# Kernel tuning notes

Measured on AMD Instinct MI355X. Metric: run time of the kernel, lower is better.

Reference implementation:

```python
import jax, jax.numpy as jnp
import numpy as np

B = 4_194_304
N_LAYERS = 2


def setup_inputs() -> dict:
    key = jax.random.key(0)
    k1, k2 = jax.random.split(key)
    x = jax.random.normal(k1, (B, 2), dtype=jnp.float32)
    q_weights = 0.01 * jax.random.normal(k2, (N_LAYERS, 2), dtype=jnp.float32)
    return {"x": x, "q_weights": q_weights}


def _apply_rx(state, theta, qubit):
    """Apply RX(theta) to `qubit` of a batched 2-qubit state [B,2,2].
    RX(t) = [[cos(t/2), -i sin(t/2)], [-i sin(t/2), cos(t/2)]].
    theta: [B] (per-sample) or scalar (shared weight)."""
    b = state.shape[0]
    theta = jnp.broadcast_to(theta, (b,))
    c = jnp.cos(0.5 * theta)[:, None].astype(state.dtype)
    s = (-1j * jnp.sin(0.5 * theta))[:, None].astype(state.dtype)
    if qubit == 0:
        a0, a1 = state[:, 0, :], state[:, 1, :]
        return jnp.stack([c * a0 + s * a1, s * a0 + c * a1], axis=1)
    else:
        a0, a1 = state[:, :, 0], state[:, :, 1]
        return jnp.stack([c * a0 + s * a1, s * a0 + c * a1], axis=2)


def _cnot01(state):
    # control = qubit0, target = qubit1: swap target amps where control == 1
    return jnp.stack([state[:, 0, :], state[:, 1, ::-1]], axis=1)


def reference(x, q_weights):
    b = x.shape[0]
    # |00> initial state, batched: [B, 2, 2] (axes = qubit0, qubit1)
    state = jnp.zeros((b, 2, 2), dtype=jnp.complex64).at[:, 0, 0].set(1.0)
    # AngleEmbedding (default rotation = RX) with per-sample angles
    state = _apply_rx(state, x[:, 0], 0)
    state = _apply_rx(state, x[:, 1], 1)
    # BasicEntanglerLayers: per layer RX on each wire, then single CNOT(0,1)
    for l in range(q_weights.shape[0]):
        state = _apply_rx(state, q_weights[l, 0], 0)
        state = _apply_rx(state, q_weights[l, 1], 1)
        state = _cnot01(state)
    # <Z_0> = P(qubit0=0) - P(qubit0=1)
    probs = jnp.real(state * jnp.conj(state))
    expz0 = jnp.sum(probs[:, 0, :], axis=-1) - jnp.sum(probs[:, 1, :], axis=-1)
    return (0.5 * (expz0 + 1.0)).astype(jnp.float32).reshape(-1, 1)
```

## Files before the change

kernel.cpp:

```cpp
#include <hip/hip_runtime.h>
#include <math.h>

#define N_LAYERS 2

typedef float vfloat4 __attribute__((ext_vector_type(4)));

__device__ __forceinline__ void rx_pair(float2& a, float2& b, float c, float s) {
    float2 na = make_float2(fmaf(c, a.x,  s * b.y), fmaf(c, a.y, -s * b.x));
    float2 nb = make_float2(fmaf(s, a.y,  c * b.x), fmaf(-s, a.x, c * b.y));
    a = na; b = nb;
}

__device__ void compute_K(const float* __restrict__ w, float* __restrict__ K) {
    float2 U[4][4];
    for (int j = 0; j < 4; ++j)
        for (int r = 0; r < 4; ++r)
            U[j][r] = make_float2(j == r ? 1.f : 0.f, 0.f);

    for (int l = 0; l < N_LAYERS; ++l) {
        float t0 = 0.5f * w[2 * l + 0];
        float t1 = 0.5f * w[2 * l + 1];
        float c0 = __cosf(t0), s0 = __sinf(t0);
        float c1 = __cosf(t1), s1 = __sinf(t1);
        for (int j = 0; j < 4; ++j) {
            rx_pair(U[j][0], U[j][2], c0, s0);
            rx_pair(U[j][1], U[j][3], c0, s0);
            rx_pair(U[j][0], U[j][1], c1, s1);
            rx_pair(U[j][2], U[j][3], c1, s1);
            float2 tmp = U[j][2]; U[j][2] = U[j][3]; U[j][3] = tmp;
        }
    }

    float Mre[4][4], Mim[4][4];
    for (int j = 0; j < 4; ++j)
        for (int k = 0; k < 4; ++k) {
            float re = 0.f, im = 0.f;
            for (int m = 0; m < 2; ++m) {
                re += U[j][m].x * U[k][m].x + U[j][m].y * U[k][m].y;
                im += U[j][m].x * U[k][m].y - U[j][m].y * U[k][m].x;
            }
            Mre[j][k] = re; Mim[j][k] = im;
        }

    float N00 = Mre[0][0], N11 = Mre[1][1], N22 = Mre[2][2], N33 = Mre[3][3];
    float N01 = Mim[0][1], N23 = Mim[2][3], N02 = Mim[0][2], N13 = Mim[1][3];
    float N03 = -Mre[0][3], N12 = Mre[1][2];

    K[0] = 0.25f * (N00 + N11 + N22 + N33);
    K[1] = 0.25f * (N00 - N11 + N22 - N33);
    K[2] = 0.50f * (N01 + N23);
    K[3] = 0.25f * (N00 + N11 - N22 - N33);
    K[4] = 0.25f * (N00 - N11 - N22 + N33);
    K[5] = 0.50f * (N01 - N23);
    K[6] = 0.50f * (N02 + N13);
    K[7] = 0.50f * (N02 - N13);
    K[8] = 0.50f * (N03 + N12);
}

__global__ __launch_bounds__(64) void qnet_coef_kernel(const float* __restrict__ w,
                                                       float* __restrict__ K) {
    if (threadIdx.x == 0) {
        float Kl[9];
        compute_K(w, Kl);
        #pragma unroll
        for (int j = 0; j < 9; ++j) K[j] = Kl[j];
    }
}

__device__ __forceinline__ float qnet_eval1(float x0, float x1,
                                            float k0, float k1, float k2,
                                            float k3, float k4, float k5,
                                            float k6, float k7, float k8) {
    float X0, S0, X1, S1;
    __sincosf(x0, &S0, &X0);
    __sincosf(x1, &S1, &X1);
    float t0 = fmaf(k2, S1, fmaf(k1, X1, k0));
    float t1 = fmaf(k5, S1, fmaf(k4, X1, k3));
    float t2 = fmaf(k8, S1, fmaf(k7, X1, k6));
    return fmaf(S0, t2, fmaf(X0, t1, t0));
}

__global__ __launch_bounds__(256, 4) void qnet_eval_kernel(
    const float4* __restrict__ x, const float* __restrict__ Kg,
    vfloat4* __restrict__ out, int nquads) {
    const float k0 = Kg[0], k1 = Kg[1], k2 = Kg[2],
                k3 = Kg[3], k4 = Kg[4], k5 = Kg[5],
                k6 = Kg[6], k7 = Kg[7], k8 = Kg[8];

    int i = blockIdx.x * blockDim.x + threadIdx.x;
    int q0 = 2 * i;
    if (q0 + 1 < nquads) {
        float4 xa = x[2 * q0 + 0];
        float4 xb = x[2 * q0 + 1];
        float4 xc = x[2 * q0 + 2];
        float4 xd = x[2 * q0 + 3];
        vfloat4 r0, r1;
        r0.x = qnet_eval1(xa.x, xa.y, k0, k1, k2, k3, k4, k5, k6, k7, k8);
        r0.y = qnet_eval1(xa.z, xa.w, k0, k1, k2, k3, k4, k5, k6, k7, k8);
        r0.z = qnet_eval1(xb.x, xb.y, k0, k1, k2, k3, k4, k5, k6, k7, k8);
        r0.w = qnet_eval1(xb.z, xb.w, k0, k1, k2, k3, k4, k5, k6, k7, k8);
        r1.x = qnet_eval1(xc.x, xc.y, k0, k1, k2, k3, k4, k5, k6, k7, k8);
        r1.y = qnet_eval1(xc.z, xc.w, k0, k1, k2, k3, k4, k5, k6, k7, k8);
        r1.z = qnet_eval1(xd.x, xd.y, k0, k1, k2, k3, k4, k5, k6, k7, k8);
        r1.w = qnet_eval1(xd.z, xd.w, k0, k1, k2, k3, k4, k5, k6, k7, k8);
        __builtin_nontemporal_store(r0, &out[q0 + 0]);
        __builtin_nontemporal_store(r1, &out[q0 + 1]);
    } else if (q0 < nquads) {
        float4 xa = x[2 * q0 + 0];
        float4 xb = x[2 * q0 + 1];
        vfloat4 r0;
        r0.x = qnet_eval1(xa.x, xa.y, k0, k1, k2, k3, k4, k5, k6, k7, k8);
        r0.y = qnet_eval1(xa.z, xa.w, k0, k1, k2, k3, k4, k5, k6, k7, k8);
        r0.z = qnet_eval1(xb.x, xb.y, k0, k1, k2, k3, k4, k5, k6, k7, k8);
        r0.w = qnet_eval1(xb.z, xb.w, k0, k1, k2, k3, k4, k5, k6, k7, k8);
        __builtin_nontemporal_store(r0, &out[q0]);
    }
}

extern "C" void kernel_launch(void* const* d_in, const int* in_sizes, int n_in,
                              void* d_out, int out_size, void* d_ws, size_t ws_size,
                              hipStream_t stream) {
    const float* x = (const float*)d_in[0];
    const float* w = (const float*)d_in[1];
    float* K = (float*)d_ws;

    qnet_coef_kernel<<<1, 64, 0, stream>>>(w, K);

    int nquads = in_sizes[0] / 8;
    int nthreads = (nquads + 1) / 2;
    int blocks = (nthreads + 255) / 256;
    qnet_eval_kernel<<<blocks, 256, 0, stream>>>(
        (const float4*)x, K, (vfloat4*)d_out, nquads);
}
```

Baseline: 80.08 us.

## Fuse coefficient computation into eval kernel, computing K per block in shared memory

Removes the separate single-thread coefficient kernel launch and instead has thread 0 of every block compute the 9 folded coefficients into shared memory, followed by a block barrier. Input loads are issued before the barrier so memory latency overlaps the serial coefficient computation. This saves a kernel launch and the launch-to-launch dependency gap, but every block (about 8K of them) now redundantly runs the serial unitary/coefficient math in one lane while the others wait. The launch_bounds occupancy hint is also relaxed.

```diff
diff --git a/kernel.cpp b/kernel.cpp
--- a/kernel.cpp
+++ b/kernel.cpp
@@ -57,16 +57,6 @@
     K[8] = 0.50f * (N03 + N12);
 }
 
-__global__ __launch_bounds__(64) void qnet_coef_kernel(const float* __restrict__ w,
-                                                       float* __restrict__ K) {
-    if (threadIdx.x == 0) {
-        float Kl[9];
-        compute_K(w, Kl);
-        #pragma unroll
-        for (int j = 0; j < 9; ++j) K[j] = Kl[j];
-    }
-}
-
 __device__ __forceinline__ float qnet_eval1(float x0, float x1,
                                             float k0, float k1, float k2,
                                             float k3, float k4, float k5,
@@ -80,20 +70,33 @@
     return fmaf(S0, t2, fmaf(X0, t1, t0));
 }
 
-__global__ __launch_bounds__(256, 4) void qnet_eval_kernel(
-    const float4* __restrict__ x, const float* __restrict__ Kg,
+__global__ __launch_bounds__(256) void qnet_fused_kernel(
+    const float4* __restrict__ x, const float* __restrict__ w,
     vfloat4* __restrict__ out, int nquads) {
-    const float k0 = Kg[0], k1 = Kg[1], k2 = Kg[2],
-                k3 = Kg[3], k4 = Kg[4], k5 = Kg[5],
-                k6 = Kg[6], k7 = Kg[7], k8 = Kg[8];
-
     int i = blockIdx.x * blockDim.x + threadIdx.x;
     int q0 = 2 * i;
-    if (q0 + 1 < nquads) {
-        float4 xa = x[2 * q0 + 0];
-        float4 xb = x[2 * q0 + 1];
-        float4 xc = x[2 * q0 + 2];
-        float4 xd = x[2 * q0 + 3];
+    bool full = (q0 + 1 < nquads);
+    bool tail = (q0 < nquads);
+
+    float4 xa, xb, xc, xd;
+    if (tail) {
+        xa = x[2 * q0 + 0];
+        xb = x[2 * q0 + 1];
+    }
+    if (full) {
+        xc = x[2 * q0 + 2];
+        xd = x[2 * q0 + 3];
+    }
+
+    __shared__ float Ks[9];
+    if (threadIdx.x == 0) compute_K(w, Ks);
+    __syncthreads();
+
+    float k0 = Ks[0], k1 = Ks[1], k2 = Ks[2];
+    float k3 = Ks[3], k4 = Ks[4], k5 = Ks[5];
+    float k6 = Ks[6], k7 = Ks[7], k8 = Ks[8];
+
+    if (full) {
         vfloat4 r0, r1;
         r0.x = qnet_eval1(xa.x, xa.y, k0, k1, k2, k3, k4, k5, k6, k7, k8);
         r0.y = qnet_eval1(xa.z, xa.w, k0, k1, k2, k3, k4, k5, k6, k7, k8);
@@ -105,9 +108,7 @@
         r1.w = qnet_eval1(xd.z, xd.w, k0, k1, k2, k3, k4, k5, k6, k7, k8);
         __builtin_nontemporal_store(r0, &out[q0 + 0]);
         __builtin_nontemporal_store(r1, &out[q0 + 1]);
-    } else if (q0 < nquads) {
-        float4 xa = x[2 * q0 + 0];
-        float4 xb = x[2 * q0 + 1];
+    } else if (tail) {
         vfloat4 r0;
         r0.x = qnet_eval1(xa.x, xa.y, k0, k1, k2, k3, k4, k5, k6, k7, k8);
         r0.y = qnet_eval1(xa.z, xa.w, k0, k1, k2, k3, k4, k5, k6, k7, k8);
@@ -122,13 +123,10 @@
                               hipStream_t stream) {
     const float* x = (const float*)d_in[0];
     const float* w = (const float*)d_in[1];
-    float* K = (float*)d_ws;
-
-    qnet_coef_kernel<<<1, 64, 0, stream>>>(w, K);
 
     int nquads = in_sizes[0] / 8;
     int nthreads = (nquads + 1) / 2;
     int blocks = (nthreads + 255) / 256;
-    qnet_eval_kernel<<<blocks, 256, 0, stream>>>(
-        (const float4*)x, K, (vfloat4*)d_out, nquads);
+    qnet_fused_kernel<<<blocks, 256, 0, stream>>>(
+        (const float4*)x, w, (vfloat4*)d_out, nquads);
 }
```

After: 78.30 us. 1.02x faster.
